# Kernel optimization log

Hardware: AMD Instinct MI355X
Metric: run time of the kernel (lower is better)

## Reference

```python
import jax, jax.numpy as jnp
import numpy as np

BATCH, SEQ, IN_DIM, OUT_DIM, N_STATE = 16, 4096, 64, 64, 512


def setup_inputs() -> dict:
    key = jax.random.key(0)
    k_x, k_a, k_b, k_c, k_d = jax.random.split(key, 5)
    x = jax.random.normal(k_x, (BATCH, SEQ, IN_DIM), dtype=jnp.float32)
    # Stable transition matrix: spectral-norm-ish scaling keeps h bounded over SEQ steps.
    A = jax.random.normal(k_a, (N_STATE, N_STATE), dtype=jnp.float32) * (0.9 / np.sqrt(N_STATE))
    B = jax.random.normal(k_b, (N_STATE, IN_DIM), dtype=jnp.float32) / np.sqrt(IN_DIM)
    C = jax.random.normal(k_c, (OUT_DIM, N_STATE), dtype=jnp.float32) / np.sqrt(N_STATE)
    D = jax.random.normal(k_d, (OUT_DIM, IN_DIM), dtype=jnp.float32) / np.sqrt(IN_DIM)
    return {"x": x, "A": A, "B": B, "C": C, "D": D}


def reference(x, A, B, C, D):
    """Linear SSM recurrence: h_t = A h_{t-1} + B x_t ; y_t = C h_t + D x_t.

    x: [batch, seq, in_dim] -> y: [batch, seq, out_dim]
    """
    batch = x.shape[0]
    n = A.shape[0]
    # Precompute input projections once (batched GEMMs outside the scan).
    bx = jnp.einsum("ni,bsi->sbn", B, x)   # [seq, batch, n_state]
    dx = jnp.einsum("oi,bsi->bso", D, x)   # [batch, seq, out_dim]

    def step(h, bx_t):
        # h: [batch, n_state]; bx_t: [batch, n_state]
        h_new = h @ A.T + bx_t
        return h_new, h_new

    h0 = jnp.zeros((batch, n), dtype=x.dtype)
    _, hs = jax.lax.scan(step, h0, bx)      # hs: [seq, batch, n_state]
    y = jnp.einsum("on,sbn->bso", C, hs) + dx
    return y
```

## Files before the change

### kernel.cpp

```cpp
#include <hip/hip_runtime.h>
#include <cstdint>
#include <cstddef>

#define BATCH 16
#define SEQ   4096
#define NS    512
#define TLAG  128
#define CTILE 256
#define XROWS (CTILE + TLAG - 1)
#define XSTR  72
#define BLK   32768

typedef unsigned short u16;
typedef unsigned int   u32;
typedef short bf16x8 __attribute__((ext_vector_type(8)));
typedef float f32x4  __attribute__((ext_vector_type(4)));

__device__ __forceinline__ u16 f2bf(float f) {
    u32 u = __builtin_bit_cast(u32, f);
    return (u16)((u + 0x7FFFu + ((u >> 16) & 1u)) >> 16);
}
__device__ __forceinline__ float bf2f(u16 h) {
    return __builtin_bit_cast(float, (u32)h << 16);
}

__global__ __launch_bounds__(256) void prep_mat(const float* __restrict__ A,
                                                const float* __restrict__ B,
                                                const float* __restrict__ C,
                                                u16* __restrict__ Arm,
                                                u16* __restrict__ At,
                                                u16* __restrict__ Rt,
                                                u16* __restrict__ L)
{
    const int id = blockIdx.x * 256 + threadIdx.x;
    if (id < 262144) {
        const int c = id & 511;
        const u16 v = f2bf(A[id]);
        Arm[id] = v;
        At[(size_t)c * 512 + (id >> 9)] = v;
    } else if (id < 262144 + 32768) {
        const int i = id - 262144;
        Rt[(size_t)(i & 63) * 512 + (i >> 6)] = f2bf(B[i]);
    } else {
        const int i = id - 262144 - 32768;
        L[i] = f2bf(C[i]);
    }
}

__device__ __forceinline__ void gemm_tile(const u16* __restrict__ apM,
                                          const u16* __restrict__ bT, int n0,
                                          u16* __restrict__ oRM,
                                          u16* __restrict__ oT, int rowT,
                                          u16* __restrict__ lds)
{
    const int tid = threadIdx.x;
    const int w = tid >> 6, l = tid & 63;
    const int lr = l & 15, q8 = (l >> 4) * 8;

    const u16* ap  = apM + (size_t)(w * 16 + lr) * NS + q8;
    const u16* bp0 = bT  + (size_t)(n0 + lr) * NS + q8;

    f32x4 acc[4];
    const f32x4 zero = {0.f, 0.f, 0.f, 0.f};
    #pragma unroll
    for (int nt = 0; nt < 4; ++nt) acc[nt] = zero;

    #pragma unroll 4
    for (int ks = 0; ks < 16; ++ks) {
        const bf16x8 a = *(const bf16x8*)(ap + ks * 32);
        #pragma unroll
        for (int nt = 0; nt < 4; ++nt) {
            const bf16x8 bfr = *(const bf16x8*)(bp0 + (size_t)nt * 16 * NS + ks * 32);
            acc[nt] = __builtin_amdgcn_mfma_f32_16x16x32_bf16(a, bfr, acc[nt], 0, 0, 0);
        }
    }

    const int rr = (l >> 4) * 4;
    if (oT) {
        #pragma unroll
        for (int nt = 0; nt < 4; ++nt) {
            const int col = n0 + nt * 16 + lr;
            ushort4 pk;
            pk.x = f2bf(acc[nt][0]); pk.y = f2bf(acc[nt][1]);
            pk.z = f2bf(acc[nt][2]); pk.w = f2bf(acc[nt][3]);
            *(ushort4*)(oT + (size_t)col * NS + rowT + w * 16 + rr) = pk;
        }
    }
    if (oRM) {
        #pragma unroll
        for (int nt = 0; nt < 4; ++nt)
            #pragma unroll
            for (int r = 0; r < 4; ++r)
                lds[(w * 16 + rr + r) * 72 + nt * 16 + lr] = f2bf(acc[nt][r]);
        __syncthreads();
        const int r  = tid >> 2;
        const int c0 = (tid & 3) * 16;
        #pragma unroll
        for (int k = 0; k < 4; ++k) {
            const ushort4 q = *(const ushort4*)&lds[r * 72 + c0 + k * 4];
            *(ushort4*)(oRM + (size_t)r * NS + n0 + c0 + k * 4) = q;
        }
    }
}

__global__ __launch_bounds__(256, 1) void stage_kernel(const u16* __restrict__ expAp,
                                                       const u16* __restrict__ expBT,
                                                       u16* __restrict__ expOut,
                                                       const u16* __restrict__ sqIn,
                                                       const u16* __restrict__ sqInT,
                                                       u16* __restrict__ sqOutRM,
                                                       u16* __restrict__ sqOutT,
                                                       int E)
{
    __shared__ u16 lds[64 * 72];
    const int t = blockIdx.x;
    if (t < E) {
        const int j = t >> 3, n0 = (t & 7) * 64;
        gemm_tile(expAp + (size_t)j * BLK, expBT, n0,
                  expOut + (size_t)j * BLK, nullptr, 0, lds);
    } else {
        const int tt = t - E;
        const int mr = tt >> 3, n0 = (tt & 7) * 64;
        gemm_tile(sqIn + (size_t)mr * BLK, sqInT, n0,
                  sqOutRM + (size_t)mr * BLK, sqOutT, mr * 64, lds);
    }
}

__global__ __launch_bounds__(256, 1) void g_kernel(const u16* __restrict__ Rt,
                                                   const u16* __restrict__ L,
                                                   const float* __restrict__ D,
                                                   u16* __restrict__ Gsw)
{
    __shared__ u16 lds[64 * 72];
    const int m = blockIdx.x;
    const int q = m >> 4, r = m & 15;
    const u16* ap0 = Rt + (size_t)q * BLK;
    const u16* bT0 = L  + (size_t)r * BLK;

    const int tid = threadIdx.x;
    const int w = tid >> 6, l = tid & 63;
    const int lr = l & 15, q8 = (l >> 4) * 8;

    const u16* ap  = ap0 + (size_t)(w * 16 + lr) * NS + q8;
    const u16* bp0 = bT0 + (size_t)lr * NS + q8;

    f32x4 acc[4];
    const f32x4 zero = {0.f, 0.f, 0.f, 0.f};
    #pragma unroll
    for (int nt = 0; nt < 4; ++nt) acc[nt] = zero;

    #pragma unroll 4
    for (int ks = 0; ks < 16; ++ks) {
        const bf16x8 a = *(const bf16x8*)(ap + ks * 32);
        #pragma unroll
        for (int nt = 0; nt < 4; ++nt) {
            const bf16x8 bfr = *(const bf16x8*)(bp0 + (size_t)nt * 16 * NS + ks * 32);
            acc[nt] = __builtin_amdgcn_mfma_f32_16x16x32_bf16(a, bfr, acc[nt], 0, 0, 0);
        }
    }

    const int rr = (l >> 4) * 4;
    #pragma unroll
    for (int nt = 0; nt < 4; ++nt)
        #pragma unroll
        for (int rk = 0; rk < 4; ++rk)
            lds[(nt * 16 + lr) * 72 + (w * 16 + rr + rk)] = f2bf(acc[nt][rk]);
    __syncthreads();

    const int f = tid >> 6;
    #pragma unroll
    for (int f2 = 0; f2 < 8; f2 += 4) {
        const int fi = f2 + f;
        const int ks = fi >> 2, nt = fi & 3;
        const int o  = nt * 16 + (l & 15);
        const int i0 = ks * 32 + (l >> 4) * 8;
        u16 v[8];
        #pragma unroll
        for (int j = 0; j < 8; ++j) {
            u16 gv = lds[o * 72 + i0 + j];
            if (m == 0) gv = f2bf(bf2f(gv) + D[o * 64 + i0 + j]);
            v[j] = gv;
        }
        ushort4 p0; p0.x = v[0]; p0.y = v[1]; p0.z = v[2]; p0.w = v[3];
        ushort4 p1; p1.x = v[4]; p1.y = v[5]; p1.z = v[6]; p1.w = v[7];
        u16* dst = Gsw + ((size_t)(m * 8 + fi) * 64 + l) * 8;
        *(ushort4*)(dst + 0) = p0;
        *(ushort4*)(dst + 4) = p1;
    }
}

__global__ __launch_bounds__(256, 1) void conv_kernel(const float* __restrict__ x,
                                                      const u16* __restrict__ gsw,
                                                      float* __restrict__ y)
{
    __shared__ u16 Xs[XROWS * XSTR];
    __shared__ uint4 Gs[2][1024];

    const int tid = threadIdx.x;
    const int b  = blockIdx.y;
    const int t0 = blockIdx.x * CTILE;

    {
        const int g = tid & 15;
        int r = tid >> 4;
        #pragma unroll
        for (int it = 0; it < 24; ++it, r += 16) {
            if (r < XROWS) {
                const int t = t0 + r - (TLAG - 1);
                ushort4 o;
                if (t < 0) {
                    o.x = 0; o.y = 0; o.z = 0; o.w = 0;
                } else {
                    const float4 v = *(const float4*)(x + ((size_t)b * SEQ + t) * 64 + g * 4);
                    o.x = f2bf(v.x); o.y = f2bf(v.y); o.z = f2bf(v.z); o.w = f2bf(v.w);
                }
                *(ushort4*)&Xs[r * XSTR + g * 4] = o;
            }
        }
    }

    const uint4* gp4 = (const uint4*)gsw;
    uint4 st[4];
    #pragma unroll
    for (int j = 0; j < 4; ++j) st[j] = gp4[tid + j * 256];

    const int w    = tid >> 6;
    const int l    = tid & 63;
    const int lr   = l & 15;
    const int q8   = (l >> 4) * 8;
    const int wrow = w * 64;

    f32x4 acc[4][4];
    const f32x4 zero = {0.f, 0.f, 0.f, 0.f};
    #pragma unroll
    for (int mt = 0; mt < 4; ++mt)
        #pragma unroll
        for (int nt = 0; nt < 4; ++nt) acc[mt][nt] = zero;

    #pragma unroll
    for (int j = 0; j < 4; ++j) Gs[0][tid + j * 256] = st[j];
    __syncthreads();

    for (int p = 0; p < 64; ++p) {
        const int cur = p & 1;
        if (p < 63) {
            #pragma unroll
            for (int j = 0; j < 4; ++j) st[j] = gp4[(p + 1) * 1024 + tid + j * 256];
        }
        #pragma unroll
        for (int sub = 0; sub < 2; ++sub) {
            const int m = 2 * p + sub;
            bf16x8 bc[8];
            #pragma unroll
            for (int f = 0; f < 8; ++f)
                bc[f] = __builtin_bit_cast(bf16x8, Gs[cur][sub * 512 + f * 64 + l]);

            const int rbase = wrow + lr + (TLAG - 1) - m;
            bf16x8 a[4][2];
            #pragma unroll
            for (int mt = 0; mt < 4; ++mt)
                #pragma unroll
                for (int ks = 0; ks < 2; ++ks)
                    a[mt][ks] = *(const bf16x8*)&Xs[(rbase + mt * 16) * XSTR + ks * 32 + q8];

            #pragma unroll
            for (int ks = 0; ks < 2; ++ks)
                #pragma unroll
                for (int mt = 0; mt < 4; ++mt)
                    #pragma unroll
                    for (int nt = 0; nt < 4; ++nt)
                        acc[mt][nt] = __builtin_amdgcn_mfma_f32_16x16x32_bf16(
                            a[mt][ks], bc[ks * 4 + nt], acc[mt][nt], 0, 0, 0);
        }
        if (p < 63) {
            #pragma unroll
            for (int j = 0; j < 4; ++j) Gs[cur ^ 1][tid + j * 256] = st[j];
        }
        __syncthreads();
    }

    const int rr = (l >> 4) * 4;
    #pragma unroll
    for (int mt = 0; mt < 4; ++mt) {
        #pragma unroll
        for (int nt = 0; nt < 4; ++nt) {
            const int t = t0 + wrow + mt * 16 + rr;
            const int o = nt * 16 + lr;
            float* yp = y + ((size_t)b * SEQ + t) * 64 + o;
            #pragma unroll
            for (int r = 0; r < 4; ++r) yp[(size_t)r * 64] = acc[mt][nt][r];
        }
    }
}

extern "C" void kernel_launch(void* const* d_in, const int* in_sizes, int n_in,
                              void* d_out, int out_size, void* d_ws, size_t ws_size,
                              hipStream_t stream)
{
    const float* x = (const float*)d_in[0];
    const float* A = (const float*)d_in[1];
    const float* B = (const float*)d_in[2];
    const float* C = (const float*)d_in[3];
    const float* D = (const float*)d_in[4];
    float* y = (float*)d_out;

    char* w = (char*)d_ws;
    u16* Arm   = (u16*)(w + 8650752);
    u16* At    = (u16*)(w + 9175040);
    u16* A2rm  = (u16*)(w + 9699328);
    u16* A2t   = (u16*)(w + 10223616);
    u16* A4rm  = (u16*)(w + 10747904);
    u16* A4t   = (u16*)(w + 11272192);
    u16* A8rm  = (u16*)(w + 11796480);
    u16* A8t   = (u16*)(w + 12320768);
    u16* A16rm = (u16*)(w + 12845056);
    u16* A16t  = (u16*)(w + 13369344);
    u16* A32rm = (u16*)(w + 13893632);
    u16* A32t  = (u16*)(w + 14417920);
    u16* A64rm = (u16*)(w + 14942208);
    u16* L     = (u16*)(w + 15532032);
    u16* Rt    = (u16*)(w + 16580608);
    u16* Gsw   = (u16*)(w + 17104896);

    prep_mat<<<1280, 256, 0, stream>>>(A, B, C, Arm, At, Rt, L);

    stage_kernel<<<72, 256, 0, stream>>>(L, At, L + 1 * BLK,
                                         Arm, At, A2rm, A2t, 8);
    stage_kernel<<<80, 256, 0, stream>>>(L, A2t, L + 2 * BLK,
                                         A2rm, A2t, A4rm, A4t, 16);
    stage_kernel<<<96, 256, 0, stream>>>(L, A4t, L + 4 * BLK,
                                         A4rm, A4t, A8rm, A8t, 32);
    stage_kernel<<<128, 256, 0, stream>>>(L, A8t, L + 8 * BLK,
                                          A8rm, A8t, A16rm, A16t, 64);
    stage_kernel<<<72, 256, 0, stream>>>(Rt, A16rm, Rt + 1 * BLK,
                                         A16rm, A16t, A32rm, A32t, 8);
    stage_kernel<<<80, 256, 0, stream>>>(Rt, A32rm, Rt + 2 * BLK,
                                         A32rm, A32t, A64rm, nullptr, 16);
    stage_kernel<<<32, 256, 0, stream>>>(Rt, A64rm, Rt + 4 * BLK,
                                         nullptr, nullptr, nullptr, nullptr, 32);
    g_kernel<<<128, 256, 0, stream>>>(Rt, L, D, Gsw);

    conv_kernel<<<dim3(SEQ / CTILE, BATCH), 256, 0, stream>>>(x, Gsw, y);
}
```

Measured before the change: 255.8 us.

## Fuse matrix-power chain into one persistent kernel with grid barriers; halve conv tile

Replaces the prep kernel, seven stage launches and the G kernel with a single persistent 128-block kernel. Its phases are separated by atomic-counter grid barriers, and intermediate results are written with agent-scope atomic stores so other blocks can see them. This is meant to remove the launch gaps between many small dependent GEMM stages. Separately, the conv kernel tile shrinks from 256 to 128 time steps with two blocks per CU, giving more blocks and better occupancy. The grid barrier relies on all 128 blocks being co-resident, has a timeout break that could silently skip the wait, and uses only relaxed ordering, so correctness depends on these assumptions.

```diff
diff --git a/kernel.cpp b/kernel.cpp
--- a/kernel.cpp
+++ b/kernel.cpp
@@ -6,13 +6,15 @@
 #define SEQ   4096
 #define NS    512
 #define TLAG  128
-#define CTILE 256
+#define CTILE 128
 #define XROWS (CTILE + TLAG - 1)
 #define XSTR  72
 #define BLK   32768
+#define NB    128
 
 typedef unsigned short u16;
 typedef unsigned int   u32;
+typedef unsigned long long u64;
 typedef short bf16x8 __attribute__((ext_vector_type(8)));
 typedef float f32x4  __attribute__((ext_vector_type(4)));
 
@@ -24,34 +26,30 @@
     return __builtin_bit_cast(float, (u32)h << 16);
 }
 
-__global__ __launch_bounds__(256) void prep_mat(const float* __restrict__ A,
-                                                const float* __restrict__ B,
-                                                const float* __restrict__ C,
-                                                u16* __restrict__ Arm,
-                                                u16* __restrict__ At,
-                                                u16* __restrict__ Rt,
-                                                u16* __restrict__ L)
-{
-    const int id = blockIdx.x * 256 + threadIdx.x;
-    if (id < 262144) {
-        const int c = id & 511;
-        const u16 v = f2bf(A[id]);
-        Arm[id] = v;
-        At[(size_t)c * 512 + (id >> 9)] = v;
-    } else if (id < 262144 + 32768) {
-        const int i = id - 262144;
-        Rt[(size_t)(i & 63) * 512 + (i >> 6)] = f2bf(B[i]);
-    } else {
-        const int i = id - 262144 - 32768;
-        L[i] = f2bf(C[i]);
-    }
-}
-
-__device__ __forceinline__ void gemm_tile(const u16* __restrict__ apM,
-                                          const u16* __restrict__ bT, int n0,
-                                          u16* __restrict__ oRM,
-                                          u16* __restrict__ oT, int rowT,
-                                          u16* __restrict__ lds)
+__device__ __forceinline__ void wt_store(u16* p, ushort4 v) {
+    __hip_atomic_store((u64*)p, __builtin_bit_cast(u64, v),
+                       __ATOMIC_RELAXED, __HIP_MEMORY_SCOPE_AGENT);
+}
+
+__device__ __forceinline__ void gbar(u32* __restrict__ f)
+{
+    __syncthreads();
+    if (threadIdx.x == 0) {
+        __hip_atomic_fetch_add(f, 1u, __ATOMIC_RELAXED, __HIP_MEMORY_SCOPE_AGENT);
+        u32 it = 0;
+        while (__hip_atomic_load(f, __ATOMIC_RELAXED, __HIP_MEMORY_SCOPE_AGENT) < (u32)NB) {
+            __builtin_amdgcn_s_sleep(8);
+            if (++it > 2000000u) break;
+        }
+    }
+    __syncthreads();
+}
+
+__device__ __forceinline__ void gemm_wt(const u16* __restrict__ apM,
+                                        const u16* __restrict__ bT, int n0,
+                                        u16* __restrict__ oRM,
+                                        u16* __restrict__ oT, int rowT,
+                                        u16* __restrict__ lds)
 {
     const int tid = threadIdx.x;
     const int w = tid >> 6, l = tid & 63;
@@ -76,67 +74,41 @@
     }
 
     const int rr = (l >> 4) * 4;
-    if (oT) {
-        #pragma unroll
-        for (int nt = 0; nt < 4; ++nt) {
-            const int col = n0 + nt * 16 + lr;
-            ushort4 pk;
-            pk.x = f2bf(acc[nt][0]); pk.y = f2bf(acc[nt][1]);
-            pk.z = f2bf(acc[nt][2]); pk.w = f2bf(acc[nt][3]);
-            *(ushort4*)(oT + (size_t)col * NS + rowT + w * 16 + rr) = pk;
-        }
-    }
+    __syncthreads();
+    #pragma unroll
+    for (int nt = 0; nt < 4; ++nt)
+        #pragma unroll
+        for (int r = 0; r < 4; ++r)
+            lds[(w * 16 + rr + r) * 72 + nt * 16 + lr] = f2bf(acc[nt][r]);
+    __syncthreads();
+
     if (oRM) {
-        #pragma unroll
-        for (int nt = 0; nt < 4; ++nt)
-            #pragma unroll
-            for (int r = 0; r < 4; ++r)
-                lds[(w * 16 + rr + r) * 72 + nt * 16 + lr] = f2bf(acc[nt][r]);
-        __syncthreads();
         const int r  = tid >> 2;
         const int c0 = (tid & 3) * 16;
         #pragma unroll
-        for (int k = 0; k < 4; ++k) {
-            const ushort4 q = *(const ushort4*)&lds[r * 72 + c0 + k * 4];
-            *(ushort4*)(oRM + (size_t)r * NS + n0 + c0 + k * 4) = q;
-        }
-    }
-}
-
-__global__ __launch_bounds__(256, 1) void stage_kernel(const u16* __restrict__ expAp,
-                                                       const u16* __restrict__ expBT,
-                                                       u16* __restrict__ expOut,
-                                                       const u16* __restrict__ sqIn,
-                                                       const u16* __restrict__ sqInT,
-                                                       u16* __restrict__ sqOutRM,
-                                                       u16* __restrict__ sqOutT,
-                                                       int E)
-{
-    __shared__ u16 lds[64 * 72];
-    const int t = blockIdx.x;
-    if (t < E) {
-        const int j = t >> 3, n0 = (t & 7) * 64;
-        gemm_tile(expAp + (size_t)j * BLK, expBT, n0,
-                  expOut + (size_t)j * BLK, nullptr, 0, lds);
-    } else {
-        const int tt = t - E;
-        const int mr = tt >> 3, n0 = (tt & 7) * 64;
-        gemm_tile(sqIn + (size_t)mr * BLK, sqInT, n0,
-                  sqOutRM + (size_t)mr * BLK, sqOutT, mr * 64, lds);
-    }
-}
-
-__global__ __launch_bounds__(256, 1) void g_kernel(const u16* __restrict__ Rt,
-                                                   const u16* __restrict__ L,
-                                                   const float* __restrict__ D,
-                                                   u16* __restrict__ Gsw)
-{
-    __shared__ u16 lds[64 * 72];
-    const int m = blockIdx.x;
-    const int q = m >> 4, r = m & 15;
-    const u16* ap0 = Rt + (size_t)q * BLK;
-    const u16* bT0 = L  + (size_t)r * BLK;
-
+        for (int k = 0; k < 4; ++k)
+            wt_store(oRM + (size_t)r * NS + n0 + c0 + k * 4,
+                     *(const ushort4*)&lds[r * 72 + c0 + k * 4]);
+    }
+    if (oT) {
+        const int col = tid >> 2;
+        const int rs  = (tid & 3) * 16;
+        u16 v[16];
+        #pragma unroll
+        for (int i = 0; i < 16; ++i) v[i] = lds[(rs + i) * 72 + col];
+        #pragma unroll
+        for (int k = 0; k < 4; ++k)
+            wt_store(oT + (size_t)(n0 + col) * NS + rowT + rs + k * 4,
+                     *(const ushort4*)&v[k * 4]);
+    }
+}
+
+__device__ __forceinline__ void g_tile(const u16* __restrict__ ap0,
+                                       const u16* __restrict__ bT0, int m,
+                                       const float* __restrict__ D,
+                                       u16* __restrict__ Gsw,
+                                       u16* __restrict__ lds)
+{
     const int tid = threadIdx.x;
     const int w = tid >> 6, l = tid & 63;
     const int lr = l & 15, q8 = (l >> 4) * 8;
@@ -160,6 +132,7 @@
     }
 
     const int rr = (l >> 4) * 4;
+    __syncthreads();
     #pragma unroll
     for (int nt = 0; nt < 4; ++nt)
         #pragma unroll
@@ -181,15 +154,135 @@
             if (m == 0) gv = f2bf(bf2f(gv) + D[o * 64 + i0 + j]);
             v[j] = gv;
         }
-        ushort4 p0; p0.x = v[0]; p0.y = v[1]; p0.z = v[2]; p0.w = v[3];
-        ushort4 p1; p1.x = v[4]; p1.y = v[5]; p1.z = v[6]; p1.w = v[7];
         u16* dst = Gsw + ((size_t)(m * 8 + fi) * 64 + l) * 8;
-        *(ushort4*)(dst + 0) = p0;
-        *(ushort4*)(dst + 4) = p1;
-    }
-}
-
-__global__ __launch_bounds__(256, 1) void conv_kernel(const float* __restrict__ x,
+        wt_store(dst + 0, *(const ushort4*)&v[0]);
+        wt_store(dst + 4, *(const ushort4*)&v[4]);
+    }
+}
+
+__global__ __launch_bounds__(256, 1) void chain9(const float* __restrict__ A,
+                                                 const float* __restrict__ B,
+                                                 const float* __restrict__ C,
+                                                 const float* __restrict__ D,
+                                                 u16* __restrict__ Arm,
+                                                 u16* __restrict__ At,
+                                                 u16* __restrict__ A2rm,
+                                                 u16* __restrict__ A2t,
+                                                 u16* __restrict__ A4rm,
+                                                 u16* __restrict__ A4t,
+                                                 u16* __restrict__ A8rm,
+                                                 u16* __restrict__ A8t,
+                                                 u16* __restrict__ A16rm,
+                                                 u16* __restrict__ A16t,
+                                                 u16* __restrict__ A32rm,
+                                                 u16* __restrict__ A32t,
+                                                 u16* __restrict__ A64rm,
+                                                 u16* __restrict__ L,
+                                                 u16* __restrict__ Rt,
+                                                 u16* __restrict__ Gsw,
+                                                 u32* __restrict__ flg)
+{
+    __shared__ u16 lds[64 * 72];
+    const int tid = threadIdx.x;
+    const int bid = blockIdx.x;
+    const int gid = bid * 256 + tid;
+
+    {
+        u16 v[8];
+        {
+            const int base = gid * 8;
+            #pragma unroll
+            for (int i = 0; i < 8; ++i) v[i] = f2bf(A[base + i]);
+            wt_store(Arm + base, *(const ushort4*)&v[0]);
+            wt_store(Arm + base + 4, *(const ushort4*)&v[4]);
+        }
+        {
+            const int col = gid >> 6, r0 = (gid & 63) * 8;
+            #pragma unroll
+            for (int i = 0; i < 8; ++i) v[i] = f2bf(A[(size_t)(r0 + i) * 512 + col]);
+            wt_store(At + (size_t)col * 512 + r0, *(const ushort4*)&v[0]);
+            wt_store(At + (size_t)col * 512 + r0 + 4, *(const ushort4*)&v[4]);
+        }
+        if (gid < 4096) {
+            const int col = gid >> 6, k0 = (gid & 63) * 8;
+            #pragma unroll
+            for (int i = 0; i < 8; ++i) v[i] = f2bf(B[(size_t)(k0 + i) * 64 + col]);
+            wt_store(Rt + (size_t)col * 512 + k0, *(const ushort4*)&v[0]);
+            wt_store(Rt + (size_t)col * 512 + k0 + 4, *(const ushort4*)&v[4]);
+        }
+        if (gid < 8192) {
+            const int base = gid * 8;
+            #pragma unroll
+            for (int i = 0; i < 8; ++i) v[i] = f2bf(C[base + i]);
+            wt_store(L + base, *(const ushort4*)&v[0]);
+            wt_store(L + base + 4, *(const ushort4*)&v[4]);
+        }
+    }
+    gbar(flg + 0);
+
+    {
+        const u16* sqI[4] = {Arm, A2rm, A4rm, A8rm};
+        const u16* sqT[4] = {At,  A2t,  A4t,  A8t};
+        u16* sqOR[4] = {A2rm, A4rm, A8rm, A16rm};
+        u16* sqOT[4] = {A2t,  A4t,  A8t,  A16t};
+        #pragma unroll 1
+        for (int lvl = 0; lvl < 4; ++lvl) {
+            const int h   = 1 << lvl;
+            const int tot = 64 + 8 * h;
+            for (int t = bid; t < tot; t += NB) {
+                if (t < 64) {
+                    const int mr = t >> 3, n0 = (t & 7) * 64;
+                    gemm_wt(sqI[lvl] + (size_t)mr * BLK, sqT[lvl], n0,
+                            sqOR[lvl] + (size_t)mr * BLK, sqOT[lvl], mr * 64, lds);
+                } else {
+                    const int tt = t - 64, j = tt >> 3, n0 = (tt & 7) * 64;
+                    gemm_wt(L + (size_t)j * BLK, sqT[lvl], n0,
+                            L + (size_t)(h + j) * BLK, nullptr, 0, lds);
+                }
+            }
+            gbar(flg + 1 + lvl);
+        }
+    }
+
+    for (int t = bid; t < 64 + 8; t += NB) {
+        if (t < 64) {
+            const int mr = t >> 3, n0 = (t & 7) * 64;
+            gemm_wt(A16rm + (size_t)mr * BLK, A16t, n0,
+                    A32rm + (size_t)mr * BLK, A32t, mr * 64, lds);
+        } else {
+            const int n0 = ((t - 64) & 7) * 64;
+            gemm_wt(Rt, A16rm, n0, Rt + 1 * BLK, nullptr, 0, lds);
+        }
+    }
+    gbar(flg + 5);
+
+    for (int t = bid; t < 64 + 16; t += NB) {
+        if (t < 64) {
+            const int mr = t >> 3, n0 = (t & 7) * 64;
+            gemm_wt(A32rm + (size_t)mr * BLK, A32t, n0,
+                    A64rm + (size_t)mr * BLK, nullptr, 0, lds);
+        } else {
+            const int tt = t - 64, j = tt >> 3, n0 = (tt & 7) * 64;
+            gemm_wt(Rt + (size_t)j * BLK, A32rm, n0,
+                    Rt + (size_t)(2 + j) * BLK, nullptr, 0, lds);
+        }
+    }
+    gbar(flg + 6);
+
+    for (int t = bid; t < 32; t += NB) {
+        const int j = t >> 3, n0 = (t & 7) * 64;
+        gemm_wt(Rt + (size_t)j * BLK, A64rm, n0,
+                Rt + (size_t)(4 + j) * BLK, nullptr, 0, lds);
+    }
+    gbar(flg + 7);
+
+    for (int m = bid; m < TLAG; m += NB) {
+        g_tile(Rt + (size_t)(m >> 4) * BLK, L + (size_t)(m & 15) * BLK,
+               m, D, Gsw, lds);
+    }
+}
+
+__global__ __launch_bounds__(256, 2) void conv_kernel(const float* __restrict__ x,
                                                       const u16* __restrict__ gsw,
                                                       float* __restrict__ y)
 {
@@ -204,7 +297,7 @@
         const int g = tid & 15;
         int r = tid >> 4;
         #pragma unroll
-        for (int it = 0; it < 24; ++it, r += 16) {
+        for (int it = 0; it < 16; ++it, r += 16) {
             if (r < XROWS) {
                 const int t = t0 + r - (TLAG - 1);
                 ushort4 o;
@@ -228,12 +321,12 @@
     const int l    = tid & 63;
     const int lr   = l & 15;
     const int q8   = (l >> 4) * 8;
-    const int wrow = w * 64;
-
-    f32x4 acc[4][4];
+    const int wrow = w * 32;
+
+    f32x4 acc[2][4];
     const f32x4 zero = {0.f, 0.f, 0.f, 0.f};
     #pragma unroll
-    for (int mt = 0; mt < 4; ++mt)
+    for (int mt = 0; mt < 2; ++mt)
         #pragma unroll
         for (int nt = 0; nt < 4; ++nt) acc[mt][nt] = zero;
 
@@ -256,9 +349,9 @@
                 bc[f] = __builtin_bit_cast(bf16x8, Gs[cur][sub * 512 + f * 64 + l]);
 
             const int rbase = wrow + lr + (TLAG - 1) - m;
-            bf16x8 a[4][2];
-            #pragma unroll
-            for (int mt = 0; mt < 4; ++mt)
+            bf16x8 a[2][2];
+            #pragma unroll
+            for (int mt = 0; mt < 2; ++mt)
                 #pragma unroll
                 for (int ks = 0; ks < 2; ++ks)
                     a[mt][ks] = *(const bf16x8*)&Xs[(rbase + mt * 16) * XSTR + ks * 32 + q8];
@@ -266,7 +359,7 @@
             #pragma unroll
             for (int ks = 0; ks < 2; ++ks)
                 #pragma unroll
-                for (int mt = 0; mt < 4; ++mt)
+                for (int mt = 0; mt < 2; ++mt)
                     #pragma unroll
                     for (int nt = 0; nt < 4; ++nt)
                         acc[mt][nt] = __builtin_amdgcn_mfma_f32_16x16x32_bf16(
@@ -281,7 +374,7 @@
 
     const int rr = (l >> 4) * 4;
     #pragma unroll
-    for (int mt = 0; mt < 4; ++mt) {
+    for (int mt = 0; mt < 2; ++mt) {
         #pragma unroll
         for (int nt = 0; nt < 4; ++nt) {
             const int t = t0 + wrow + mt * 16 + rr;
@@ -321,24 +414,14 @@
     u16* L     = (u16*)(w + 15532032);
     u16* Rt    = (u16*)(w + 16580608);
     u16* Gsw   = (u16*)(w + 17104896);
-
-    prep_mat<<<1280, 256, 0, stream>>>(A, B, C, Arm, At, Rt, L);
-
-    stage_kernel<<<72, 256, 0, stream>>>(L, At, L + 1 * BLK,
-                                         Arm, At, A2rm, A2t, 8);
-    stage_kernel<<<80, 256, 0, stream>>>(L, A2t, L + 2 * BLK,
-                                         A2rm, A2t, A4rm, A4t, 16);
-    stage_kernel<<<96, 256, 0, stream>>>(L, A4t, L + 4 * BLK,
-                                         A4rm, A4t, A8rm, A8t, 32);
-    stage_kernel<<<128, 256, 0, stream>>>(L, A8t, L + 8 * BLK,
-                                          A8rm, A8t, A16rm, A16t, 64);
-    stage_kernel<<<72, 256, 0, stream>>>(Rt, A16rm, Rt + 1 * BLK,
-                                         A16rm, A16t, A32rm, A32t, 8);
-    stage_kernel<<<80, 256, 0, stream>>>(Rt, A32rm, Rt + 2 * BLK,
-                                         A32rm, A32t, A64rm, nullptr, 16);
-    stage_kernel<<<32, 256, 0, stream>>>(Rt, A64rm, Rt + 4 * BLK,
-                                         nullptr, nullptr, nullptr, nullptr, 32);
-    g_kernel<<<128, 256, 0, stream>>>(Rt, L, D, Gsw);
+    u32* flg   = (u32*)(w + 18153472);
+
+    hipMemsetAsync(flg, 0, 64, stream);
+
+    chain9<<<NB, 256, 0, stream>>>(A, B, C, D,
+                                   Arm, At, A2rm, A2t, A4rm, A4t, A8rm, A8t,
+                                   A16rm, A16t, A32rm, A32t, A64rm,
+                                   L, Rt, Gsw, flg);
 
     conv_kernel<<<dim3(SEQ / CTILE, BATCH), 256, 0, stream>>>(x, Gsw, y);
 }
```

New measurement: 273.0 us. 1.07x slower.
